# Kernel optimization log

Measured on AMD Instinct MI355X. Metric: run time of the kernel, lower is better.

Reference implementation:

```python
import jax, jax.numpy as jnp
import numpy as np

N = 128  # image size
J = 4    # number of scales
L = 4    # number of orientations


def make_morlet_filters(n, j_max, n_angles):
    """Fixed Morlet filter bank in Fourier space, shape [J, L, N, N] (real)."""
    freqs = np.fft.fftfreq(n) * 2.0 * np.pi
    kx = freqs[:, None] * np.ones((1, n))
    ky = np.ones((n, 1)) * freqs[None, :]
    filters = np.zeros((j_max, n_angles, n, n), dtype=np.float32)
    for j in range(j_max):
        k0 = 3.0 * np.pi / 4.0 / (2.0 ** j)   # central frequency of scale j
        sigma = 0.8 * (2.0 ** j)               # gaussian width in space
        for l in range(n_angles):
            theta = np.pi * l / n_angles
            k0x, k0y = k0 * np.cos(theta), k0 * np.sin(theta)
            beta = np.exp(-0.5 * sigma ** 2 * k0 ** 2)  # zero-mean correction
            g_shift = np.exp(-0.5 * sigma ** 2 * ((kx - k0x) ** 2 + (ky - k0y) ** 2))
            g_zero = np.exp(-0.5 * sigma ** 2 * (kx ** 2 + ky ** 2))
            filters[j, l] = g_shift - beta * g_zero
    return jnp.asarray(filters)


PSI = make_morlet_filters(N, J, L)  # fixed (non-learned) filter bank
VALID_PAIRS = [(j1, j2) for j1 in range(J) for j2 in range(J) if j2 > j1]  # 6 pairs


def setup_inputs() -> dict:
    key = jax.random.key(0)
    k1, k2, k3, k4, k5 = jax.random.split(key, 5)
    B = 64
    return {
        "image_batch": jax.random.normal(k1, (B, N, N), dtype=jnp.float32),
        "fc1_w": jax.random.normal(k2, (4, 11), dtype=jnp.float32) * 0.3,
        "fc1_b": jax.random.normal(k3, (4,), dtype=jnp.float32) * 0.1,
        "fc2_w": jax.random.normal(k4, (10, 4), dtype=jnp.float32) * 0.3,
        "fc2_b": jax.random.normal(k5, (10,), dtype=jnp.float32) * 0.1,
    }


def _scattering(image):
    # image: [B, N, N]
    i_hat = jnp.fft.fft2(image)  # [B,N,N] complex64
    s0 = jnp.mean(image, axis=(1, 2))  # [B]
    # first order: |x * psi_{j1,l1}|  -> [B,J,L,N,N]
    u1 = jnp.abs(jnp.fft.ifft2(i_hat[:, None, None] * PSI[None]))
    s1 = jnp.mean(u1, axis=(2, 3, 4))  # [B,J] averaged over orientations+space
    u1_hat = jnp.fft.fft2(u1)  # [B,J,L,N,N]
    # second order: only j2 > j1 (others NaN in original and masked out)
    s2_list = []
    for (j1, j2) in VALID_PAIRS:
        # [B, L1, L2, N, N]
        field = jnp.fft.ifft2(u1_hat[:, j1, :, None] * PSI[j2][None, None])
        s2_list.append(jnp.mean(jnp.abs(field), axis=(1, 2, 3, 4)))
    s2 = jnp.stack(s2_list, axis=1)  # [B,6]
    return jnp.concatenate([s0[:, None], s1, s2], axis=1)  # [B,11]


def reference(image_batch, fc1_w, fc1_b, fc2_w, fc2_b):
    coeffs = _scattering(image_batch)                      # [B,11]
    h = jax.nn.relu(coeffs @ fc1_w.T + fc1_b)              # [B,4]
    return jax.nn.sigmoid(h @ fc2_w.T + fc2_b)             # [B,10]
```

## Files before the change

kernel.cpp:

```cpp
#include <hip/hip_runtime.h>
#include <math.h>

#define NN   128
#define SS   129
#define TT   512
#define NPIX 16384
#define EPT  32
#define SG   65
#define SG32 33


__device__ __forceinline__ float2 cmul(float2 a, float2 w) {
    return make_float2(a.x * w.x - a.y * w.y, a.x * w.y + a.y * w.x);
}
__device__ __forceinline__ float2 cmulc(float2 a, float2 w) {
    return make_float2(a.x * w.x + a.y * w.y, a.y * w.x - a.x * w.y);
}

template<int SGN>
__device__ __forceinline__ void fft4(float2* f) {
    float2 t0 = make_float2(f[0].x + f[2].x, f[0].y + f[2].y);
    float2 t1 = make_float2(f[0].x - f[2].x, f[0].y - f[2].y);
    float2 t2 = make_float2(f[1].x + f[3].x, f[1].y + f[3].y);
    float2 t3 = make_float2(f[1].x - f[3].x, f[1].y - f[3].y);
    float2 t3i = (SGN > 0) ? make_float2(-t3.y, t3.x) : make_float2(t3.y, -t3.x);
    f[0] = make_float2(t0.x + t2.x, t0.y + t2.y);
    f[1] = make_float2(t1.x + t3i.x, t1.y + t3i.y);
    f[2] = make_float2(t0.x - t2.x, t0.y - t2.y);
    f[3] = make_float2(t1.x - t3i.x, t1.y - t3i.y);
}

template<int SGN>
__device__ __forceinline__ void fft8(float2* f) {
    const float R = 0.70710678118654752f;
    const float WC[4] = {1.f, R, 0.f, -R};
    const float WS[4] = {0.f, R, 1.f, R};
    #pragma unroll
    for (int stage = 0; stage < 3; ++stage) {
        const int L = 8 >> stage, half = L >> 1, step = 1 << stage;
        #pragma unroll
        for (int base = 0; base < 8; base += L) {
            #pragma unroll
            for (int j = 0; j < half; ++j) {
                float2 u = f[base + j], v = f[base + half + j];
                f[base + j] = make_float2(u.x + v.x, u.y + v.y);
                float dx = u.x - v.x, dy = u.y - v.y;
                const int t = j * step;
                const float wr = WC[t];
                const float wi = (SGN > 0) ? WS[t] : -WS[t];
                f[base + half + j] = make_float2(dx * wr - dy * wi, dx * wi + dy * wr);
            }
        }
    }
    float2 tmp;
    tmp = f[1]; f[1] = f[4]; f[4] = tmp;
    tmp = f[3]; f[3] = f[6]; f[6] = tmp;
}

template<int SGN>
__device__ __forceinline__ void fft16(float2* f) {
    const float WC[8] = {1.f, 0.92387953251f, 0.70710678119f, 0.38268343236f,
                         0.f, -0.38268343236f, -0.70710678119f, -0.92387953251f};
    const float WS[8] = {0.f, 0.38268343236f, 0.70710678119f, 0.92387953251f,
                         1.f, 0.92387953251f, 0.70710678119f, 0.38268343236f};
    #pragma unroll
    for (int stage = 0; stage < 4; ++stage) {
        const int L = 16 >> stage, half = L >> 1, step = 1 << stage;
        #pragma unroll
        for (int base = 0; base < 16; base += L) {
            #pragma unroll
            for (int j = 0; j < half; ++j) {
                float2 u = f[base + j], v = f[base + half + j];
                f[base + j] = make_float2(u.x + v.x, u.y + v.y);
                float dx = u.x - v.x, dy = u.y - v.y;
                const int t = j * step;
                const float wr = WC[t];
                const float wi = (SGN > 0) ? WS[t] : -WS[t];
                f[base + half + j] = make_float2(dx * wr - dy * wi, dx * wi + dy * wr);
            }
        }
    }
    float2 tmp;
    tmp = f[1];  f[1]  = f[8];  f[8]  = tmp;
    tmp = f[2];  f[2]  = f[4];  f[4]  = tmp;
    tmp = f[3];  f[3]  = f[12]; f[12] = tmp;
    tmp = f[5];  f[5]  = f[10]; f[10] = tmp;
    tmp = f[7];  f[7]  = f[14]; f[14] = tmp;
    tmp = f[11]; f[11] = f[13]; f[13] = tmp;
}

__device__ __forceinline__ float waveReduceSum(float v) {
    #pragma unroll
    for (int off = 32; off > 0; off >>= 1) v += __shfl_down(v, off, 64);
    return v;
}

__device__ __forceinline__ void buildTw(float2* tw, int tid) {
    if (tid < 128) {
        float s, c;
        __sincosf((float)tid * 0.04908738521234052f, &s, &c);
        tw[tid] = make_float2(c, s);
    }
}

__device__ __forceinline__ float pass32x4(float4* __restrict__ P4a,
                                          float4* __restrict__ P4b,
                                          const float2* __restrict__ tw, int tid) {
    __syncthreads();
    {
        float4* P = (tid & 256) ? P4b : P4a;
        int line = tid & 31, a = (tid >> 5) & 7;
        float2 f0[4], f1[4];
        #pragma unroll
        for (int kb = 0; kb < 4; ++kb) {
            float4 v = P[(4 * a + kb) * SG32 + line];
            f0[kb] = make_float2(v.x, v.y); f1[kb] = make_float2(v.z, v.w);
        }
        fft4<1>(f0); fft4<1>(f1);
        #pragma unroll
        for (int t = 0; t < 4; ++t) {
            float2 w = tw[4 * t * a];
            float2 aa = cmul(f0[t], w), d = cmul(f1[t], w);
            P[(4 * a + t) * SG32 + line] = make_float4(aa.x, aa.y, d.x, d.y);
        }
    }
    __syncthreads();
    if (tid < 256) {
        float4* P = (tid & 128) ? P4b : P4a;
        int line = tid & 31, t = (tid >> 5) & 3;
        float2 f0[8], f1[8];
        #pragma unroll
        for (int a = 0; a < 8; ++a) {
            float4 v = P[(4 * a + t) * SG32 + line];
            f0[a] = make_float2(v.x, v.y); f1[a] = make_float2(v.z, v.w);
        }
        fft8<1>(f0); fft8<1>(f1);
        #pragma unroll
        for (int n1 = 0; n1 < 8; ++n1)
            P[(4 * n1 + t) * SG32 + line] =
                make_float4(f0[n1].x, f0[n1].y, f1[n1].x, f1[n1].y);
    }
    __syncthreads();
    {
        float4* P = (tid & 256) ? P4b : P4a;
        int row = tid & 31, a = (tid >> 5) & 7;
        float4* R = P + row * SG32 + 4 * a;
        float2 f0[4], f1[4];
        #pragma unroll
        for (int kb = 0; kb < 4; ++kb) {
            float4 v = R[kb];
            f0[kb] = make_float2(v.x, v.y); f1[kb] = make_float2(v.z, v.w);
        }
        fft4<1>(f0); fft4<1>(f1);
        #pragma unroll
        for (int t = 0; t < 4; ++t) {
            float2 w = tw[4 * t * a];
            float2 aa = cmul(f0[t], w), d = cmul(f1[t], w);
            R[t] = make_float4(aa.x, aa.y, d.x, d.y);
        }
    }
    __syncthreads();
    float a2 = 0.f;
    if (tid < 256) {
        float4* P = (tid & 128) ? P4b : P4a;
        int row = tid & 31, t = (tid >> 5) & 3;
        float4* R = P + row * SG32 + t;
        float2 f0[8], f1[8];
        #pragma unroll
        for (int a = 0; a < 8; ++a) {
            float4 v = R[4 * a];
            f0[a] = make_float2(v.x, v.y); f1[a] = make_float2(v.z, v.w);
        }
        fft8<1>(f0); fft8<1>(f1);
        #pragma unroll
        for (int n1 = 0; n1 < 8; ++n1) {
            a2 += sqrtf(f0[n1].x * f0[n1].x + f0[n1].y * f0[n1].y);
            a2 += sqrtf(f1[n1].x * f1[n1].x + f1[n1].y * f1[n1].y);
        }
    }
    return a2;
}

__device__ __forceinline__ void pass32combo(float2* __restrict__ Q0, float2* __restrict__ Q1,
                                            float2* __restrict__ Q2, float2* __restrict__ Q3,
                                            float4* __restrict__ Pa, float4* __restrict__ Pb,
                                            const float2* __restrict__ tw, int tid,
                                            float& aq, float& ap) {
    __syncthreads();
    {
        float2* Qx = (tid & 256) ? Q2 : Q0;
        float2* Qy = (tid & 256) ? Q3 : Q1;
        float4* P  = (tid & 256) ? Pb : Pa;
        int line = tid & 31, a = (tid >> 5) & 7;
        float2 q0[4], q1[4], f0[4], f1[4];
        #pragma unroll
        for (int kb = 0; kb < 4; ++kb) {
            int o = (4 * a + kb) * SG32 + line;
            q0[kb] = Qx[o]; q1[kb] = Qy[o];
            float4 v = P[o];
            f0[kb] = make_float2(v.x, v.y); f1[kb] = make_float2(v.z, v.w);
        }
        fft4<1>(q0); fft4<1>(q1); fft4<1>(f0); fft4<1>(f1);
        #pragma unroll
        for (int t = 0; t < 4; ++t) {
            float2 w = tw[4 * t * a];
            int o = (4 * a + t) * SG32 + line;
            Qx[o] = cmul(q0[t], w); Qy[o] = cmul(q1[t], w);
            float2 aa = cmul(f0[t], w), d = cmul(f1[t], w);
            P[o] = make_float4(aa.x, aa.y, d.x, d.y);
        }
    }
    __syncthreads();
    if (tid < 256) {
        float2* Qx = (tid & 128) ? Q2 : Q0;
        float2* Qy = (tid & 128) ? Q3 : Q1;
        float4* P  = (tid & 128) ? Pb : Pa;
        int line = tid & 31, t = (tid >> 5) & 3;
        float2 q0[8], q1[8], f0[8], f1[8];
        #pragma unroll
        for (int a = 0; a < 8; ++a) {
            int o = (4 * a + t) * SG32 + line;
            q0[a] = Qx[o]; q1[a] = Qy[o];
            float4 v = P[o];
            f0[a] = make_float2(v.x, v.y); f1[a] = make_float2(v.z, v.w);
        }
        fft8<1>(q0); fft8<1>(q1); fft8<1>(f0); fft8<1>(f1);
        #pragma unroll
        for (int n1 = 0; n1 < 8; ++n1) {
            int o = (4 * n1 + t) * SG32 + line;
            Qx[o] = q0[n1]; Qy[o] = q1[n1];
            P[o] = make_float4(f0[n1].x, f0[n1].y, f1[n1].x, f1[n1].y);
        }
    }
    __syncthreads();
    {
        float2* Qx = (tid & 256) ? Q2 : Q0;
        float2* Qy = (tid & 256) ? Q3 : Q1;
        float4* P  = (tid & 256) ? Pb : Pa;
        int row = tid & 31, a = (tid >> 5) & 7;
        int base = row * SG32 + 4 * a;
        float2 q0[4], q1[4], f0[4], f1[4];
        #pragma unroll
        for (int kb = 0; kb < 4; ++kb) {
            q0[kb] = Qx[base + kb]; q1[kb] = Qy[base + kb];
            float4 v = P[base + kb];
            f0[kb] = make_float2(v.x, v.y); f1[kb] = make_float2(v.z, v.w);
        }
        fft4<1>(q0); fft4<1>(q1); fft4<1>(f0); fft4<1>(f1);
        #pragma unroll
        for (int t = 0; t < 4; ++t) {
            float2 w = tw[4 * t * a];
            Qx[base + t] = cmul(q0[t], w); Qy[base + t] = cmul(q1[t], w);
            float2 aa = cmul(f0[t], w), d = cmul(f1[t], w);
            P[base + t] = make_float4(aa.x, aa.y, d.x, d.y);
        }
    }
    __syncthreads();
    aq = 0.f; ap = 0.f;
    if (tid < 256) {
        float2* Qx = (tid & 128) ? Q2 : Q0;
        float2* Qy = (tid & 128) ? Q3 : Q1;
        float4* P  = (tid & 128) ? Pb : Pa;
        int row = tid & 31, t = (tid >> 5) & 3;
        int base = row * SG32 + t;
        float2 q0[8], q1[8], f0[8], f1[8];
        #pragma unroll
        for (int a = 0; a < 8; ++a) {
            int o = base + 4 * a;
            q0[a] = Qx[o]; q1[a] = Qy[o];
            float4 v = P[o];
            f0[a] = make_float2(v.x, v.y); f1[a] = make_float2(v.z, v.w);
        }
        fft8<1>(q0); fft8<1>(q1); fft8<1>(f0); fft8<1>(f1);
        #pragma unroll
        for (int n1 = 0; n1 < 8; ++n1) {
            aq += sqrtf(q0[n1].x * q0[n1].x + q0[n1].y * q0[n1].y);
            aq += sqrtf(q1[n1].x * q1[n1].x + q1[n1].y * q1[n1].y);
            ap += sqrtf(f0[n1].x * f0[n1].x + f0[n1].y * f0[n1].y);
            ap += sqrtf(f1[n1].x * f1[n1].x + f1[n1].y * f1[n1].y);
        }
    }
}

template<int ES, int LS>
__device__ __forceinline__ void fwdA(float2* __restrict__ F,
                                     const float2* __restrict__ tw, int tid) {
    #pragma unroll
    for (int i = 0; i < 4; ++i) {
        int u = i * TT + tid;
        int t = u >> 7, x = u & 127;
        float2* M = F + x * LS;
        float2 f[8];
        #pragma unroll
        for (int n1 = 0; n1 < 8; ++n1) f[n1] = M[(t + 16 * n1) * ES];
        fft8<-1>(f);
        #pragma unroll
        for (int ka = 0; ka < 8; ++ka)
            M[(t + 16 * ka) * ES] = cmulc(f[ka], tw[t * ka]);
    }
}

template<int ES, int LS>
__device__ __forceinline__ void fwdB(float2* __restrict__ F, int tid) {
    #pragma unroll
    for (int i = 0; i < 2; ++i) {
        int u = i * TT + tid;
        int ka = u >> 7, x = u & 127;
        float2* M = F + x * LS;
        float2 g[16];
        #pragma unroll
        for (int t = 0; t < 16; ++t) g[t] = M[(16 * ka + t) * ES];
        fft16<-1>(g);
        #pragma unroll
        for (int kb = 0; kb < 16; ++kb) M[(16 * ka + kb) * ES] = g[kb];
    }
}

__device__ __forceinline__ void fwdB_col_capture(const float2* __restrict__ F, int tid,
                                                 float2* __restrict__ uh) {
    #pragma unroll
    for (int i = 0; i < 2; ++i) {
        int u = i * TT + tid;
        int ka = u >> 7, c = u & 127;
        float2 g[16];
        #pragma unroll
        for (int t = 0; t < 16; ++t) g[t] = F[(16 * ka + t) * SS + c];
        fft16<-1>(g);
        #pragma unroll
        for (int kb = 0; kb < 16; ++kb) uh[i * 16 + kb] = g[kb];
    }
}

template<int ES, int LS>
__device__ __forceinline__ void invA(float2* __restrict__ F,
                                     const float2* __restrict__ tw, int tid) {
    #pragma unroll
    for (int i = 0; i < 2; ++i) {
        int u = i * TT + tid;
        int ka = u >> 7, x = u & 127;
        float2* M = F + x * LS;
        float2 g[16];
        #pragma unroll
        for (int kb = 0; kb < 16; ++kb) g[kb] = M[(16 * ka + kb) * ES];
        fft16<1>(g);
        #pragma unroll
        for (int t = 0; t < 16; ++t)
            M[(16 * ka + t) * ES] = cmul(g[t], tw[t * ka]);
    }
}

template<int ES, int LS>
__device__ __forceinline__ void invB(float2* __restrict__ F, int tid) {
    #pragma unroll
    for (int i = 0; i < 4; ++i) {
        int u = i * TT + tid;
        int t = u >> 7, x = u & 127;
        float2* M = F + x * LS;
        float2 f[8];
        #pragma unroll
        for (int ka = 0; ka < 8; ++ka) f[ka] = M[(16 * ka + t) * ES];
        fft8<1>(f);
        #pragma unroll
        for (int nh = 0; nh < 8; ++nh) M[(t + 16 * nh) * ES] = f[nh];
    }
}

__device__ __forceinline__ void invBmag_fwdA_row(float2* __restrict__ F,
                                                 const float2* __restrict__ tw,
                                                 int tid, float& acc) {
    #pragma unroll
    for (int i = 0; i < 4; ++i) {
        int u = i * TT + tid;
        int t = u >> 7, x = u & 127;
        float2* M = F + x * SS;
        float2 f[8];
        #pragma unroll
        for (int ka = 0; ka < 8; ++ka) f[ka] = M[16 * ka + t];
        fft8<1>(f);
        #pragma unroll
        for (int nh = 0; nh < 8; ++nh) {
            float m = sqrtf(f[nh].x * f[nh].x + f[nh].y * f[nh].y);
            acc += m;
            f[nh] = make_float2(m, 0.f);
        }
        fft8<-1>(f);
        #pragma unroll
        for (int ka = 0; ka < 8; ++ka)
            M[t + 16 * ka] = cmulc(f[ka], tw[t * ka]);
    }
}

__global__ __attribute__((amdgpu_flat_work_group_size(TT, TT), amdgpu_waves_per_eu(2, 2)))
void k_pre(const float* __restrict__ img,
           float* __restrict__ psi,
           float2* __restrict__ ihat,
           float* __restrict__ coeffs) {
    __shared__ float2 F[NN * SS];
    __shared__ float2 tw[128];
    __shared__ float red[TT / 64];
    int blk = blockIdx.x, tid = threadIdx.x;
    if (blk >= 64) {
        if (blk == 80) {
            for (int i = tid; i < 64 * 11; i += TT)
                if (i % 11 != 0) coeffs[i] = 0.f;
            return;
        }
        int f = blk - 64;
        int j = f >> 2, l = f & 3;
        float k0    = 2.35619449019234493f / (float)(1 << j);
        float sigma = 0.8f * (float)(1 << j);
        float s2    = sigma * sigma;
        float theta = 0.78539816339744831f * (float)l;
        float k0x = k0 * cosf(theta);
        float k0y = k0 * sinf(theta);
        float beta = expf(-0.5f * s2 * k0 * k0);
        const float FSTEP = 0.04908738521234052f;
        float* dst = psi + (size_t)f * NPIX;
        for (int i = tid; i < NPIX; i += TT) {
            int pr = i >> 7, pc = i & 127;
            int kr = (pr >> 4) + 8 * (pr & 15);
            int kc = (pc >> 4) + 8 * (pc & 15);
            float fr = (float)(kr < 64 ? kr : kr - 128) * FSTEP;
            float fc = (float)(kc < 64 ? kc : kc - 128) * FSTEP;
            float dx = fr - k0x, dy = fc - k0y;
            float g1 = expf(-0.5f * s2 * (dx * dx + dy * dy));
            float g0 = expf(-0.5f * s2 * (fr * fr + fc * fc));
            dst[i] = g1 - beta * g0;
        }
        return;
    }
    int b = blk;
    buildTw(tw, tid);
    const float* im = img + (size_t)b * NPIX;
    float acc = 0.f;
    #pragma unroll
    for (int k = 0; k < EPT; ++k) {
        int e = k * TT + tid;
        float v = im[e];
        acc += v;
        F[(e >> 7) * SS + (e & 127)] = make_float2(v, 0.f);
    }
    float ws = waveReduceSum(acc);
    if ((tid & 63) == 0) red[tid >> 6] = ws;
    __syncthreads();
    if (tid == 0) {
        float t = 0.f;
        #pragma unroll
        for (int w = 0; w < TT / 64; ++w) t += red[w];
        coeffs[b * 11 + 0] = t * (1.f / 16384.f);
    }
    fwdA<1, SS>(F, tw, tid);  __syncthreads();
    fwdB<1, SS>(F, tid);      __syncthreads();
    fwdA<SS, 1>(F, tw, tid);  __syncthreads();
    float2 uh[32];
    fwdB_col_capture(F, tid, uh);
    float2* dst = ihat + (size_t)b * NPIX;
    #pragma unroll
    for (int i = 0; i < 2; ++i) {
        int u = i * TT + tid;
        int ka = u >> 7, c = u & 127;
        #pragma unroll
        for (int kb = 0; kb < 16; ++kb)
            dst[(16 * ka + kb) * NN + c] = uh[i * 16 + kb];
    }
}

__global__ __attribute__((amdgpu_flat_work_group_size(TT, TT), amdgpu_waves_per_eu(2, 2)))
void k_scat_big(const float2* __restrict__ ihat,
                const float* __restrict__ psi,
                float* __restrict__ coeffs) {
    __shared__ __align__(16) float2 F[16640];
    __shared__ float2 tw[128];
    float2* G2a = F;
    float2* G2b = F + 4160;
    float2* G2c = F + 8320;
    float2* G2d = F + 12480;
    float2* Q0 = F;
    float2* Q1 = F + 1056;
    float2* Q2 = F + 2112;
    float2* Q3 = F + 3168;
    float4* Pa = (float4*)(F + 4224);
    float4* Pb = (float4*)(F + 6336);
    int tid = threadIdx.x;
    int x = blockIdx.x;
    int b = x & 63, l1 = x >> 6;
    const float2* ih = ihat + (size_t)b * NPIX;
    const float*  p1 = psi + (size_t)l1 * NPIX;
    buildTw(tw, tid);

    const float S1_128 = 9.3132257461547852e-10f;
    const float S2TR   = 5.6843418860808015e-14f;
    const float S2_03  = 2.2737367544323206e-13f;

    int kalo = tid >> 7, c = tid & 127;
    {
        #pragma unroll
        for (int i = 0; i < 2; ++i) {
            int ka = kalo + 4 * i;
            float2 g[16];
            #pragma unroll
            for (int kb = 0; kb < 16; ++kb) {
                int e = (16 * ka + kb) * NN + c;
                float2 z = ih[e];
                float  p = p1[e];
                g[kb] = make_float2(z.x * p, z.y * p);
            }
            fft16<1>(g);
            #pragma unroll
            for (int t = 0; t < 16; ++t)
                F[(16 * ka + t) * SS + c] = cmul(g[t], tw[t * ka]);
        }
    }
    __syncthreads();
    invB<SS, 1>(F, tid);      __syncthreads();
    invA<1, SS>(F, tw, tid);  __syncthreads();
    float acc = 0.f;
    invBmag_fwdA_row(F, tw, tid, acc);
    float ws1 = waveReduceSum(acc);
    if ((tid & 63) == 0) atomicAdd(&coeffs[b * 11 + 1], ws1 * S1_128);
    __syncthreads();
    fwdB<1, SS>(F, tid);      __syncthreads();
    fwdA<SS, 1>(F, tw, tid);  __syncthreads();
    float2 uh[32];
    fwdB_col_capture(F, tid, uh);
    __syncthreads();

    int m = c & 15;
    int fc = (c >> 4) + 8 * (c & 15);

    {
        const int ORW[4] = {21, 15, 0, -15};
        const int OCW[4] = { 0, 15, 21,  15};
        bool ckw[4]; int pcw[4];
        #pragma unroll
        for (int w = 0; w < 4; ++w) {
            int dc = (fc - OCW[w]) & 127;
            ckw[w] = (dc < 32) || (dc >= 96);
            int uc = (dc < 32) ? dc : (dc - 64);
            pcw[w] = 8 * (uc & 7) + (uc >> 3);
        }
        #pragma unroll
        for (int i = 0; i < 2; ++i) {
            int ka = kalo + 4 * i;
            #pragma unroll
            for (int kb = 0; kb < 16; ++kb) {
                int fr = ka + 8 * kb;
                float2 z = uh[i * 16 + kb];
                int e = (16 * ka + kb) * NN + c;
                #pragma unroll
                for (int w = 0; w < 4; ++w) {
                    if (ckw[w]) {
                        int dr = (fr - ORW[w]) & 127;
                        if (dr < 32 || dr >= 96) {
                            int ur = (dr < 32) ? dr : (dr - 64);
                            int pr = 8 * (ur & 7) + (ur >> 3);
                            float pv = psi[(size_t)(4 + w) * NPIX + e];
                            float2* G = (w == 0) ? G2a : (w == 1) ? G2b
                                       : (w == 2) ? G2c : G2d;
                            G[pr * SG + pcw[w]] = make_float2(z.x * pv, z.y * pv);
                        }
                    }
                }
            }
        }
        __syncthreads();
        {
            int col = tid & 63, k8 = tid >> 6;
            float2 f0[8], f1[8], f2[8], f3[8];
            #pragma unroll
            for (int kb = 0; kb < 8; ++kb) {
                int o = (8 * k8 + kb) * SG + col;
                f0[kb] = G2a[o]; f1[kb] = G2b[o]; f2[kb] = G2c[o]; f3[kb] = G2d[o];
            }
            fft8<1>(f0); fft8<1>(f1); fft8<1>(f2); fft8<1>(f3);
            #pragma unroll
            for (int q = 0; q < 8; ++q) {
                float2 w = tw[2 * q * k8];
                int o = (8 * k8 + q) * SG + col;
                G2a[o] = cmul(f0[q], w); G2b[o] = cmul(f1[q], w);
                G2c[o] = cmul(f2[q], w); G2d[o] = cmul(f3[q], w);
            }
        }
        __syncthreads();
        {
            int col = tid & 63, q = tid >> 6;
            float2 f0[8], f1[8], f2[8], f3[8];
            #pragma unroll
            for (int k8 = 0; k8 < 8; ++k8) {
                int o = (8 * k8 + q) * SG + col;
                f0[k8] = G2a[o]; f1[k8] = G2b[o]; f2[k8] = G2c[o]; f3[k8] = G2d[o];
            }
            fft8<1>(f0); fft8<1>(f1); fft8<1>(f2); fft8<1>(f3);
            #pragma unroll
            for (int n1 = 0; n1 < 8; ++n1) {
                int o = (8 * n1 + q) * SG + col;
                G2a[o] = f0[n1]; G2b[o] = f1[n1]; G2c[o] = f2[n1]; G2d[o] = f3[n1];
            }
        }
        __syncthreads();
        {
            int row = tid & 63, k8 = tid >> 6;
            int base = row * SG + 8 * k8;
            float2 f0[8], f1[8], f2[8], f3[8];
            #pragma unroll
            for (int kb = 0; kb < 8; ++kb) {
                f0[kb] = G2a[base + kb]; f1[kb] = G2b[base + kb];
                f2[kb] = G2c[base + kb]; f3[kb] = G2d[base + kb];
            }
            fft8<1>(f0); fft8<1>(f1); fft8<1>(f2); fft8<1>(f3);
            #pragma unroll
            for (int q = 0; q < 8; ++q) {
                float2 w = tw[2 * q * k8];
                G2a[base + q] = cmul(f0[q], w); G2b[base + q] = cmul(f1[q], w);
                G2c[base + q] = cmul(f2[q], w); G2d[base + q] = cmul(f3[q], w);
            }
        }
        __syncthreads();
        float a2 = 0.f;
        {
            int row = tid & 63, q = tid >> 6;
            int base = row * SG + q;
            float2 f0[8], f1[8], f2[8], f3[8];
            #pragma unroll
            for (int k8 = 0; k8 < 8; ++k8) {
                int o = base + 8 * k8;
                f0[k8] = G2a[o]; f1[k8] = G2b[o]; f2[k8] = G2c[o]; f3[k8] = G2d[o];
            }
            fft8<1>(f0); fft8<1>(f1); fft8<1>(f2); fft8<1>(f3);
            #pragma unroll
            for (int n1 = 0; n1 < 8; ++n1) {
                a2 += sqrtf(f0[n1].x * f0[n1].x + f0[n1].y * f0[n1].y);
                a2 += sqrtf(f1[n1].x * f1[n1].x + f1[n1].y * f1[n1].y);
                a2 += sqrtf(f2[n1].x * f2[n1].x + f2[n1].y * f2[n1].y);
                a2 += sqrtf(f3[n1].x * f3[n1].x + f3[n1].y * f3[n1].y);
            }
        }
        float ws2 = waveReduceSum(a2);
        if ((tid & 63) == 0) atomicAdd(&coeffs[b * 11 + 5 + 0], ws2 * S2TR);
        __syncthreads();
    }

    {
        const int OR2[4] = {9, 6, 0, -6};
        const int OC2[4] = {0, 6, 9,  6};
        bool ckq[4]; int pcq[4];
        #pragma unroll
        for (int w = 0; w < 4; ++w) {
            int dc = (fc - OC2[w]) & 127;
            ckq[w] = (dc < 16) || (dc >= 112);
            int f32c = (dc < 16) ? dc : (dc - 96);
            pcq[w] = 4 * (f32c & 7) + (f32c >> 3);
        }
        bool ck32 = (m < 2) || (m >= 14);
        int pc32 = 4 * (c >> 4) + ((m < 2) ? m : (m - 12));
        const float* p30 = psi + (size_t)12 * NPIX;
        #pragma unroll
        for (int i = 0; i < 2; ++i) {
            int ka = kalo + 4 * i;
            #pragma unroll
            for (int kb = 0; kb < 16; ++kb) {
                int fr = ka + 8 * kb;
                float2 z = uh[i * 16 + kb];
                int e = (16 * ka + kb) * NN + c;
                #pragma unroll
                for (int w = 0; w < 4; ++w) {
                    if (ckq[w]) {
                        int dr = (fr - OR2[w]) & 127;
                        if (dr < 16 || dr >= 112) {
                            int f32r = (dr < 16) ? dr : (dr - 96);
                            int pr = 4 * (f32r & 7) + (f32r >> 3);
                            float pv = psi[(size_t)(8 + w) * NPIX + e];
                            float2* Q = (w == 0) ? Q0 : (w == 1) ? Q1
                                       : (w == 2) ? Q2 : Q3;
                            Q[pr * SG32 + pcq[w]] = make_float2(z.x * pv, z.y * pv);
                        }
                    }
                }
                if (ck32 && (kb < 2 || kb >= 14)) {
                    int pr32 = 4 * ka + ((kb < 2) ? kb : (kb - 12));
                    float a0 = p30[e], a1 = p30[NPIX + e];
                    float a2f = p30[2 * NPIX + e], a3 = p30[3 * NPIX + e];
                    Pa[pr32 * SG32 + pc32] =
                        make_float4(z.x * a0, z.y * a0, z.x * a1, z.y * a1);
                    Pb[pr32 * SG32 + pc32] =
                        make_float4(z.x * a2f, z.y * a2f, z.x * a3, z.y * a3);
                }
            }
        }
        float aq, ap;
        pass32combo(Q0, Q1, Q2, Q3, Pa, Pb, tw, tid, aq, ap);
        float wsq = waveReduceSum(aq);
        float wsp = waveReduceSum(ap);
        if ((tid & 63) == 0) {
            atomicAdd(&coeffs[b * 11 + 5 + 1], wsq * S2_03);
            atomicAdd(&coeffs[b * 11 + 5 + 2], wsp * S2_03);
        }
    }
}

__global__ __attribute__((amdgpu_flat_work_group_size(TT, TT), amdgpu_waves_per_eu(4, 4)))
void k_scat_small(const float2* __restrict__ ihat,
                  const float* __restrict__ psi,
                  float* __restrict__ coeffs) {
    __shared__ __align__(16) float2 S[8448];
    __shared__ float2 tw[128];
    float2* G2  = S;
    float2* G32 = S;
    float4* P4a = (float4*)S;
    float4* P4b = (float4*)S + 1056;
    float2* Qs0 = S;
    float2* Qs1 = S + 1056;
    float2* Qs2 = S + 2112;
    float2* Qs3 = S + 3168;
    float4* Psa = (float4*)(S + 4224);
    float4* Psb = (float4*)(S + 6336);
    float2* H32 = S + 6144;
    int tid = threadIdx.x;
    int x = blockIdx.x;
    int b = x & 63, l1 = (x >> 6) & 3;
    int t0 = x >> 8;
    int j1 = (t0 == 0) ? 1 : (t0 + 1);
    const float2* ih = ihat + (size_t)b * NPIX;
    const float*  p1 = psi + (size_t)(j1 * 4 + l1) * NPIX;
    buildTw(tw, tid);

    const float S1_64 = 3.7252902984619141e-9f;
    const float S1_32 = 1.4901161193847656e-8f;
    const float S2_32 = 9.0949470177292824e-13f;

    int kalo = tid >> 7, c = tid & 127;

    if (t0 == 0) {
        const int OR1[4] = {21, 15, 0, -15};
        const int OC1[4] = { 0, 15, 21,  15};
        int fc = (c >> 4) + 8 * (c & 15);
        int dc = (fc - OC1[l1]) & 127;
        bool ck = (dc < 32) || (dc >= 96);
        int ucw = (dc < 32) ? dc : (dc - 64);
        int pcd = 8 * (ucw & 7) + (ucw >> 3);
        if (ck) {
            #pragma unroll
            for (int i = 0; i < 2; ++i) {
                int ka = kalo + 4 * i;
                #pragma unroll
                for (int kb = 0; kb < 16; ++kb) {
                    int fr = ka + 8 * kb;
                    int dr = (fr - OR1[l1]) & 127;
                    if (dr < 32 || dr >= 96) {
                        int ur = (dr < 32) ? dr : (dr - 64);
                        int pr = 8 * (ur & 7) + (ur >> 3);
                        int e = (16 * ka + kb) * NN + c;
                        float2 z = ih[e];
                        float  p = p1[e];
                        G2[pr * SG + pcd] = make_float2(z.x * p, z.y * p);
                    }
                }
            }
        }
        __syncthreads();
        {
            int col = tid & 63, k8 = tid >> 6;
            float2 f[8];
            #pragma unroll
            for (int kb = 0; kb < 8; ++kb) f[kb] = G2[(8 * k8 + kb) * SG + col];
            fft8<1>(f);
            #pragma unroll
            for (int q = 0; q < 8; ++q)
                G2[(8 * k8 + q) * SG + col] = cmul(f[q], tw[2 * q * k8]);
        }
        __syncthreads();
        {
            int col = tid & 63, q = tid >> 6;
            float2 f[8];
            #pragma unroll
            for (int k8 = 0; k8 < 8; ++k8) f[k8] = G2[(8 * k8 + q) * SG + col];
            fft8<1>(f);
            #pragma unroll
            for (int n1 = 0; n1 < 8; ++n1) G2[(8 * n1 + q) * SG + col] = f[n1];
        }
        __syncthreads();
        {
            int row = tid & 63, k8 = tid >> 6;
            float2* R = G2 + row * SG + 8 * k8;
            float2 f[8];
            #pragma unroll
            for (int kb = 0; kb < 8; ++kb) f[kb] = R[kb];
            fft8<1>(f);
            #pragma unroll
            for (int q = 0; q < 8; ++q) R[q] = cmul(f[q], tw[2 * q * k8]);
        }
        __syncthreads();
        float acc = 0.f;
        {
            int row = tid & 63, q = tid >> 6;
            float2* R = G2 + row * SG + q;
            float2 f[8];
            #pragma unroll
            for (int k8 = 0; k8 < 8; ++k8) f[k8] = R[8 * k8];
            fft8<1>(f);
            #pragma unroll
            for (int n1 = 0; n1 < 8; ++n1) {
                float mg = sqrtf(f[n1].x * f[n1].x + f[n1].y * f[n1].y);
                acc += mg;
                f[n1] = make_float2(mg, 0.f);
            }
            fft8<-1>(f);
            #pragma unroll
            for (int ka = 0; ka < 8; ++ka)
                R[8 * ka] = cmulc(f[ka], tw[2 * q * ka]);
        }
        float ws1 = waveReduceSum(acc);
        if ((tid & 63) == 0) atomicAdd(&coeffs[b * 11 + 2], ws1 * S1_64);
        __syncthreads();
        {
            int row2 = tid & 63, ka = tid >> 6;
            float2* R2 = G2 + row2 * SG + 8 * ka;
            float2 g[8];
            #pragma unroll
            for (int t = 0; t < 8; ++t) g[t] = R2[t];
            fft8<-1>(g);
            #pragma unroll
            for (int kb = 0; kb < 8; ++kb) R2[kb] = g[kb];
        }
        __syncthreads();
        {
            int col = tid & 63, t = tid >> 6;
            float2 g[8];
            #pragma unroll
            for (int n1 = 0; n1 < 8; ++n1) g[n1] = G2[(t + 8 * n1) * SG + col];
            fft8<-1>(g);
            #pragma unroll
            for (int ka = 0; ka < 8; ++ka)
                G2[(t + 8 * ka) * SG + col] = cmulc(g[ka], tw[2 * t * ka]);
        }
        __syncthreads();
        float2 vh[8];
        int c6 = tid & 63, ka8 = tid >> 6;
        {
            float2 g[8];
            #pragma unroll
            for (int t = 0; t < 8; ++t) g[t] = G2[(8 * ka8 + t) * SG + c6];
            fft8<-1>(g);
            #pragma unroll
            for (int kb = 0; kb < 8; ++kb) vh[kb] = g[kb];
        }
        __syncthreads();

        int uc64 = 8 * (c6 & 7) + (c6 >> 3);
        int fc128 = (uc64 < 32) ? uc64 : (uc64 + 64);
        int scI = 16 * (fc128 & 7) + (fc128 >> 3);
        int se[8];
        #pragma unroll
        for (int kb = 0; kb < 8; ++kb) {
            int ur = 8 * kb + ka8;
            int fr128 = (ur < 32) ? ur : (ur + 64);
            se[kb] = (16 * (fr128 & 7) + (fr128 >> 3)) * NN + scI;
        }

        {
            const int OR2[4] = {9, 6, 0, -6};
            const int OC2[4] = {0, 6, 9,  6};
            bool ckq[4]; int pcq[4];
            #pragma unroll
            for (int w = 0; w < 4; ++w) {
                int dcw = (uc64 - OC2[w]) & 63;
                ckq[w] = (dcw < 16) || (dcw >= 48);
                int f32c = (dcw < 16) ? dcw : (dcw - 32);
                pcq[w] = 4 * (f32c & 7) + (f32c >> 3);
            }
            int m6 = c6 & 7;
            bool ckV = (m6 < 2) || (m6 >= 6);
            int p32c = 4 * (c6 >> 3) + ((m6 < 2) ? m6 : (m6 - 4));
            const float* p30 = psi + (size_t)12 * NPIX;
            #pragma unroll
            for (int kb = 0; kb < 8; ++kb) {
                int ur = 8 * kb + ka8;
                float2 z = vh[kb];
                int e = se[kb];
                #pragma unroll
                for (int w = 0; w < 4; ++w) {
                    if (ckq[w]) {
                        int dr = (ur - OR2[w]) & 63;
                        if (dr < 16 || dr >= 48) {
                            int f32r = (dr < 16) ? dr : (dr - 32);
                            int pr = 4 * (f32r & 7) + (f32r >> 3);
                            float pv = psi[(size_t)(8 + w) * NPIX + e];
                            float2* Q = (w == 0) ? Qs0 : (w == 1) ? Qs1
                                       : (w == 2) ? Qs2 : Qs3;
                            Q[pr * SG32 + pcq[w]] = make_float2(z.x * pv, z.y * pv);
                        }
                    }
                }
                if (ckV && (kb < 2 || kb >= 6)) {
                    int pr32 = 4 * ka8 + (kb & 3);
                    float a0 = p30[e], a1 = p30[NPIX + e];
                    float a2f = p30[2 * NPIX + e], a3 = p30[3 * NPIX + e];
                    Psa[pr32 * SG32 + p32c] =
                        make_float4(z.x * a0, z.y * a0, z.x * a1, z.y * a1);
                    Psb[pr32 * SG32 + p32c] =
                        make_float4(z.x * a2f, z.y * a2f, z.x * a3, z.y * a3);
                }
            }
            float aq, ap;
            pass32combo(Qs0, Qs1, Qs2, Qs3, Psa, Psb, tw, tid, aq, ap);
            float wsq = waveReduceSum(aq);
            float wsp = waveReduceSum(ap);
            if ((tid & 63) == 0) {
                atomicAdd(&coeffs[b * 11 + 5 + 3], wsq * S2_32);
                atomicAdd(&coeffs[b * 11 + 5 + 4], wsp * S2_32);
            }
        }
        return;
    }

    if (t0 == 2) {
        int m = c & 15;
        bool ck32 = (m < 2) || (m >= 14);
        int pc32 = 4 * (c >> 4) + ((m < 2) ? m : (m - 12));
        if (ck32) {
            #pragma unroll
            for (int i = 0; i < 2; ++i) {
                int ka = kalo + 4 * i;
                #pragma unroll
                for (int kb = 0; kb < 16; ++kb) {
                    if (kb < 2 || kb >= 14) {
                        int e = (16 * ka + kb) * NN + c;
                        float2 z = ih[e];
                        float  p = p1[e];
                        int pr32 = 4 * ka + ((kb < 2) ? kb : (kb - 12));
                        G32[pr32 * SG32 + pc32] = make_float2(z.x * p, z.y * p);
                    }
                }
            }
        }
        __syncthreads();
        if (tid < 256) {
            int line = tid & 31, a = tid >> 5;
            float2 f[4];
            #pragma unroll
            for (int kb = 0; kb < 4; ++kb) f[kb] = G32[(4 * a + kb) * SG32 + line];
            fft4<1>(f);
            #pragma unroll
            for (int t = 0; t < 4; ++t)
                G32[(4 * a + t) * SG32 + line] = cmul(f[t], tw[4 * t * a]);
        }
        __syncthreads();
        if (tid < 128) {
            int line = tid & 31, t = tid >> 5;
            float2 f[8];
            #pragma unroll
            for (int a = 0; a < 8; ++a) f[a] = G32[(4 * a + t) * SG32 + line];
            fft8<1>(f);
            #pragma unroll
            for (int n1 = 0; n1 < 8; ++n1) G32[(4 * n1 + t) * SG32 + line] = f[n1];
        }
        __syncthreads();
        if (tid < 256) {
            int row = tid & 31, a = tid >> 5;
            float2* R = G32 + row * SG32 + 4 * a;
            float2 f[4];
            #pragma unroll
            for (int kb = 0; kb < 4; ++kb) f[kb] = R[kb];
            fft4<1>(f);
            #pragma unroll
            for (int t = 0; t < 4; ++t) R[t] = cmul(f[t], tw[4 * t * a]);
        }
        __syncthreads();
        float acc = 0.f;
        if (tid < 128) {
            int row = tid & 31, t = tid >> 5;
            float2* R = G32 + row * SG32 + t;
            float2 f[8];
            #pragma unroll
            for (int a = 0; a < 8; ++a) f[a] = R[4 * a];
            fft8<1>(f);
            #pragma unroll
            for (int n1 = 0; n1 < 8; ++n1)
                acc += sqrtf(f[n1].x * f[n1].x + f[n1].y * f[n1].y);
        }
        float ws1 = waveReduceSum(acc);
        if ((tid & 63) == 0 && tid < 128) atomicAdd(&coeffs[b * 11 + 4], ws1 * S1_32);
        return;
    }

    int m = c & 15;
    bool colKeep = (m < 4) || (m >= 12);
    if (colKeep) {
        #pragma unroll
        for (int i = 0; i < 2; ++i) {
            int ka = kalo + 4 * i;
            #pragma unroll
            for (int kb = 0; kb < 16; ++kb) {
                if (kb < 4 || kb >= 12) {
                    int e = (16 * ka + kb) * NN + c;
                    float2 z = ih[e];
                    float  p = p1[e];
                    int pr64 = 8 * ka + ((kb < 4) ? kb : (kb - 8));
                    int pc64 = 8 * (c >> 4) + ((m < 4) ? m : (m - 8));
                    G2[pr64 * SG + pc64] = make_float2(z.x * p, z.y * p);
                }
            }
        }
    }
    __syncthreads();
    {
        int col = tid & 63, k8 = tid >> 6;
        float2 f[8];
        #pragma unroll
        for (int kb = 0; kb < 8; ++kb) f[kb] = G2[(8 * k8 + kb) * SG + col];
        fft8<1>(f);
        #pragma unroll
        for (int q = 0; q < 8; ++q)
            G2[(8 * k8 + q) * SG + col] = cmul(f[q], tw[2 * q * k8]);
    }
    __syncthreads();
    {
        int col = tid & 63, q = tid >> 6;
        float2 f[8];
        #pragma unroll
        for (int k8 = 0; k8 < 8; ++k8) f[k8] = G2[(8 * k8 + q) * SG + col];
        fft8<1>(f);
        #pragma unroll
        for (int n1 = 0; n1 < 8; ++n1) G2[(8 * n1 + q) * SG + col] = f[n1];
    }
    __syncthreads();
    {
        int row = tid & 63, k8 = tid >> 6;
        float2* R = G2 + row * SG + 8 * k8;
        float2 f[8];
        #pragma unroll
        for (int kb = 0; kb < 8; ++kb) f[kb] = R[kb];
        fft8<1>(f);
        #pragma unroll
        for (int q = 0; q < 8; ++q) R[q] = cmul(f[q], tw[2 * q * k8]);
    }
    __syncthreads();
    float acc = 0.f;
    {
        int row = tid & 63, q = tid >> 6;
        float2* R = G2 + row * SG + q;
        float2 f[8];
        #pragma unroll
        for (int k8 = 0; k8 < 8; ++k8) f[k8] = R[8 * k8];
        fft8<1>(f);
        #pragma unroll
        for (int n1 = 0; n1 < 8; ++n1) {
            float mg = sqrtf(f[n1].x * f[n1].x + f[n1].y * f[n1].y);
            acc += mg;
            f[n1] = make_float2(mg, 0.f);
        }
        fft8<-1>(f);
        #pragma unroll
        for (int ka = 0; ka < 8; ++ka)
            R[8 * ka] = cmulc(f[ka], tw[2 * q * ka]);
    }
    float ws1 = waveReduceSum(acc);
    if ((tid & 63) == 0) atomicAdd(&coeffs[b * 11 + 3], ws1 * S1_64);
    __syncthreads();
    {
        int row2 = tid & 63, ka = tid >> 6;
        float2* R2 = G2 + row2 * SG + 8 * ka;
        float2 g[8];
        #pragma unroll
        for (int t = 0; t < 8; ++t) g[t] = R2[t];
        fft8<-1>(g);
        #pragma unroll
        for (int kb = 0; kb < 8; ++kb) R2[kb] = g[kb];
    }
    __syncthreads();
    {
        int col = tid & 63, t = tid >> 6;
        float2 g[8];
        #pragma unroll
        for (int n1 = 0; n1 < 8; ++n1) g[n1] = G2[(t + 8 * n1) * SG + col];
        fft8<-1>(g);
        #pragma unroll
        for (int ka = 0; ka < 8; ++ka)
            G2[(t + 8 * ka) * SG + col] = cmulc(g[ka], tw[2 * t * ka]);
    }
    __syncthreads();
    {
        int col = tid & 63, ka = tid >> 6;
        float2 g[8];
        #pragma unroll
        for (int t = 0; t < 8; ++t) g[t] = G2[(8 * ka + t) * SG + col];
        fft8<-1>(g);
        int br = col & 7, ar = col >> 3;
        if (br < 2 || br >= 6) {
            int p32row = 4 * ar + (br & 3);
            #pragma unroll
            for (int kb = 0; kb < 8; ++kb) {
                if (kb < 2 || kb >= 6)
                    H32[(4 * ka + (kb & 3)) * 32 + p32row] = g[kb];
            }
        }
    }
    __syncthreads();

    {
        bool ck32 = (m < 2) || (m >= 14);
        int pc32 = 4 * (c >> 4) + ((m < 2) ? m : (m - 12));
        const float* p0 = psi + (size_t)12 * NPIX;
        const float* pq1 = p0 + NPIX;
        const float* pq2 = pq1 + NPIX;
        const float* pq3 = pq2 + NPIX;
        if (ck32) {
            #pragma unroll
            for (int i = 0; i < 2; ++i) {
                int ka = kalo + 4 * i;
                #pragma unroll
                for (int kb = 0; kb < 16; ++kb) {
                    if (kb < 2 || kb >= 14) {
                        int pr32 = 4 * ka + ((kb < 2) ? kb : (kb - 12));
                        float2 z = H32[pr32 * 32 + pc32];
                        int e = (16 * ka + kb) * NN + c;
                        float a0 = p0[e], a1 = pq1[e], a2f = pq2[e], a3 = pq3[e];
                        P4a[pr32 * SG32 + pc32] =
                            make_float4(z.x * a0, z.y * a0, z.x * a1, z.y * a1);
                        P4b[pr32 * SG32 + pc32] =
                            make_float4(z.x * a2f, z.y * a2f, z.x * a3, z.y * a3);
                    }
                }
            }
        }
        float a2 = pass32x4(P4a, P4b, tw, tid);
        float ws2 = waveReduceSum(a2);
        if ((tid & 63) == 0) atomicAdd(&coeffs[b * 11 + 5 + 5], ws2 * S2_32);
    }
}

__global__ void k_mlp(const float* __restrict__ coeffs,
                      const float* __restrict__ w1, const float* __restrict__ b1,
                      const float* __restrict__ w2, const float* __restrict__ b2,
                      float* __restrict__ out) {
    int b = threadIdx.x;
    if (b >= 64) return;
    float c[11];
    #pragma unroll
    for (int i = 0; i < 11; ++i) c[i] = coeffs[b * 11 + i];
    float h[4];
    #pragma unroll
    for (int k = 0; k < 4; ++k) {
        float s = b1[k];
        #pragma unroll
        for (int i = 0; i < 11; ++i) s += w1[k * 11 + i] * c[i];
        h[k] = fmaxf(s, 0.f);
    }
    #pragma unroll
    for (int o = 0; o < 10; ++o) {
        float s = b2[o];
        #pragma unroll
        for (int k = 0; k < 4; ++k) s += w2[o * 4 + k] * h[k];
        out[b * 10 + o] = 1.f / (1.f + expf(-s));
    }
}

extern "C" void kernel_launch(void* const* d_in, const int* in_sizes, int n_in,
                              void* d_out, int out_size, void* d_ws, size_t ws_size,
                              hipStream_t stream) {
    const float* img = (const float*)d_in[0];
    const float* w1  = (const float*)d_in[1];
    const float* b1  = (const float*)d_in[2];
    const float* w2  = (const float*)d_in[3];
    const float* b2  = (const float*)d_in[4];
    float* out = (float*)d_out;

    float*  ws     = (float*)d_ws;
    float*  psi    = ws;
    float2* ihat   = (float2*)(ws + 16 * NPIX);
    float*  coeffs = ws + 16 * NPIX + 2 * 64 * NPIX;

    hipLaunchKernelGGL(k_pre,        dim3(81),  dim3(TT), 0, stream, img, psi, ihat, coeffs);
    hipLaunchKernelGGL(k_scat_big,   dim3(256), dim3(TT), 0, stream, ihat, psi, coeffs);
    hipLaunchKernelGGL(k_scat_small, dim3(768), dim3(TT), 0, stream, ihat, psi, coeffs);
    hipLaunchKernelGGL(k_mlp,        dim3(1),   dim3(64), 0, stream, coeffs, w1, b1, w2, b2, out);
}
```

Baseline: 182.6 us.

## Split image FFT into row and column kernels and use 64x64 pass for j2=2

The single 64-block forward FFT pre-kernel becomes two kernels, each running 256 blocks over 32-row or 32-column strips. Row FFTs are staged through global memory between them, which spreads the initial FFT across more CUs. The mean coefficient s0 now comes from the DC bin of the FFT, so the separate reduction is gone. In k_scat_big, the second-order j2=2 pair switches from four shifted 32x32 windows to one 64x64 cropped window processing all four orientations together, trading extra FFT work for simpler scatter and fewer bank conflicts.

```diff
diff --git a/kernel.cpp b/kernel.cpp
--- a/kernel.cpp
+++ b/kernel.cpp
@@ -391,21 +391,19 @@
 }
 
 __global__ __attribute__((amdgpu_flat_work_group_size(TT, TT), amdgpu_waves_per_eu(2, 2)))
-void k_pre(const float* __restrict__ img,
-           float* __restrict__ psi,
-           float2* __restrict__ ihat,
-           float* __restrict__ coeffs) {
-    __shared__ float2 F[NN * SS];
+void k_pre1(const float* __restrict__ img,
+            float* __restrict__ psi,
+            float2* __restrict__ interm,
+            float* __restrict__ coeffs) {
+    __shared__ __align__(16) float2 F[32 * SS];
     __shared__ float2 tw[128];
-    __shared__ float red[TT / 64];
     int blk = blockIdx.x, tid = threadIdx.x;
-    if (blk >= 64) {
-        if (blk == 80) {
-            for (int i = tid; i < 64 * 11; i += TT)
-                if (i % 11 != 0) coeffs[i] = 0.f;
+    if (blk >= 256) {
+        if (blk == 272) {
+            for (int i = tid; i < 64 * 11; i += TT) coeffs[i] = 0.f;
             return;
         }
-        int f = blk - 64;
+        int f = blk - 256;
         int j = f >> 2, l = f & 3;
         float k0    = 2.35619449019234493f / (float)(1 << j);
         float sigma = 0.8f * (float)(1 << j);
@@ -429,39 +427,85 @@
         }
         return;
     }
-    int b = blk;
+    int b = blk >> 2, q = blk & 3;
     buildTw(tw, tid);
-    const float* im = img + (size_t)b * NPIX;
-    float acc = 0.f;
-    #pragma unroll
-    for (int k = 0; k < EPT; ++k) {
+    const float* im = img + (size_t)b * NPIX + (size_t)q * 32 * NN;
+    #pragma unroll
+    for (int k = 0; k < 8; ++k) {
         int e = k * TT + tid;
-        float v = im[e];
-        acc += v;
-        F[(e >> 7) * SS + (e & 127)] = make_float2(v, 0.f);
-    }
-    float ws = waveReduceSum(acc);
-    if ((tid & 63) == 0) red[tid >> 6] = ws;
-    __syncthreads();
-    if (tid == 0) {
-        float t = 0.f;
-        #pragma unroll
-        for (int w = 0; w < TT / 64; ++w) t += red[w];
-        coeffs[b * 11 + 0] = t * (1.f / 16384.f);
-    }
-    fwdA<1, SS>(F, tw, tid);  __syncthreads();
-    fwdB<1, SS>(F, tid);      __syncthreads();
-    fwdA<SS, 1>(F, tw, tid);  __syncthreads();
-    float2 uh[32];
-    fwdB_col_capture(F, tid, uh);
-    float2* dst = ihat + (size_t)b * NPIX;
-    #pragma unroll
-    for (int i = 0; i < 2; ++i) {
-        int u = i * TT + tid;
-        int ka = u >> 7, c = u & 127;
+        F[(e >> 7) * SS + (e & 127)] = make_float2(im[e], 0.f);
+    }
+    __syncthreads();
+    {
+        int x = tid & 31, t = tid >> 5;
+        float2* M = F + x * SS;
+        float2 f[8];
+        #pragma unroll
+        for (int n1 = 0; n1 < 8; ++n1) f[n1] = M[t + 16 * n1];
+        fft8<-1>(f);
+        #pragma unroll
+        for (int ka = 0; ka < 8; ++ka)
+            M[t + 16 * ka] = cmulc(f[ka], tw[t * ka]);
+    }
+    __syncthreads();
+    if (tid < 256) {
+        int x = tid & 31, ka = tid >> 5;
+        float2* M = F + x * SS + 16 * ka;
+        float2 g[16];
+        #pragma unroll
+        for (int t = 0; t < 16; ++t) g[t] = M[t];
+        fft16<-1>(g);
+        #pragma unroll
+        for (int kb = 0; kb < 16; ++kb) M[kb] = g[kb];
+    }
+    __syncthreads();
+    float2* dst = interm + (size_t)b * NPIX + (size_t)q * 32 * NN;
+    #pragma unroll
+    for (int k = 0; k < 8; ++k) {
+        int e = k * TT + tid;
+        dst[e] = F[(e >> 7) * SS + (e & 127)];
+    }
+}
+
+__global__ __attribute__((amdgpu_flat_work_group_size(TT, TT), amdgpu_waves_per_eu(2, 2)))
+void k_pre2(float2* __restrict__ ihat,
+            float* __restrict__ coeffs) {
+    __shared__ __align__(16) float2 F[128 * 33];
+    __shared__ float2 tw[128];
+    int blk = blockIdx.x, tid = threadIdx.x;
+    int b = blk >> 2, q = blk & 3;
+    buildTw(tw, tid);
+    float2* base = ihat + (size_t)b * NPIX + q * 32;
+    #pragma unroll
+    for (int k = 0; k < 8; ++k) {
+        int e = k * TT + tid;
+        int r = e >> 5, cl = e & 31;
+        F[r * 33 + cl] = base[r * NN + cl];
+    }
+    __syncthreads();
+    {
+        int cl = tid & 31, t = tid >> 5;
+        float2 f[8];
+        #pragma unroll
+        for (int n1 = 0; n1 < 8; ++n1) f[n1] = F[(t + 16 * n1) * 33 + cl];
+        fft8<-1>(f);
+        #pragma unroll
+        for (int ka = 0; ka < 8; ++ka)
+            F[(t + 16 * ka) * 33 + cl] = cmulc(f[ka], tw[t * ka]);
+    }
+    __syncthreads();
+    if (tid < 256) {
+        int cl = tid & 31, ka = tid >> 5;
+        float2 g[16];
+        #pragma unroll
+        for (int t = 0; t < 16; ++t) g[t] = F[(16 * ka + t) * 33 + cl];
+        fft16<-1>(g);
+        float2* dst = base + cl;
         #pragma unroll
         for (int kb = 0; kb < 16; ++kb)
-            dst[(16 * ka + kb) * NN + c] = uh[i * 16 + kb];
+            dst[(16 * ka + kb) * NN] = g[kb];
+        if (q == 0 && cl == 0 && ka == 0)
+            coeffs[b * 11 + 0] = g[0].x * (1.f / 16384.f);
     }
 }
 
@@ -471,16 +515,14 @@
                 float* __restrict__ coeffs) {
     __shared__ __align__(16) float2 F[16640];
     __shared__ float2 tw[128];
+    float4* G4a = (float4*)F;
+    float4* G4b = (float4*)(F + 8320);
     float2* G2a = F;
     float2* G2b = F + 4160;
     float2* G2c = F + 8320;
     float2* G2d = F + 12480;
-    float2* Q0 = F;
-    float2* Q1 = F + 1056;
-    float2* Q2 = F + 2112;
-    float2* Q3 = F + 3168;
-    float4* Pa = (float4*)(F + 4224);
-    float4* Pb = (float4*)(F + 6336);
+    float4* P4a = (float4*)F;
+    float4* P4b = (float4*)F + 1056;
     int tid = threadIdx.x;
     int x = blockIdx.x;
     int b = x & 63, l1 = x >> 6;
@@ -526,6 +568,8 @@
     __syncthreads();
 
     int m = c & 15;
+    bool colKeep = (m < 4) || (m >= 12);
+    int pc64 = 8 * (c >> 4) + ((m < 4) ? m : (m - 8));
     int fc = (c >> 4) + 8 * (c & 15);
 
     {
@@ -641,60 +685,150 @@
     }
 
     {
-        const int OR2[4] = {9, 6, 0, -6};
-        const int OC2[4] = {0, 6, 9,  6};
-        bool ckq[4]; int pcq[4];
-        #pragma unroll
-        for (int w = 0; w < 4; ++w) {
-            int dc = (fc - OC2[w]) & 127;
-            ckq[w] = (dc < 16) || (dc >= 112);
-            int f32c = (dc < 16) ? dc : (dc - 96);
-            pcq[w] = 4 * (f32c & 7) + (f32c >> 3);
-        }
+        const float* p0 = psi + (size_t)8 * NPIX;
+        const float* pq1 = p0 + NPIX;
+        const float* pq2 = pq1 + NPIX;
+        const float* pq3 = pq2 + NPIX;
+        if (colKeep) {
+            #pragma unroll
+            for (int i = 0; i < 2; ++i) {
+                int ka = kalo + 4 * i;
+                #pragma unroll
+                for (int kb = 0; kb < 16; ++kb) {
+                    if (kb < 4 || kb >= 12) {
+                        int pr64 = 8 * ka + ((kb < 4) ? kb : (kb - 8));
+                        float2 z = uh[i * 16 + kb];
+                        int e = (16 * ka + kb) * NN + c;
+                        float a0 = p0[e], a1 = pq1[e], a2f = pq2[e], a3 = pq3[e];
+                        G4a[pr64 * SG + pc64] =
+                            make_float4(z.x * a0, z.y * a0, z.x * a1, z.y * a1);
+                        G4b[pr64 * SG + pc64] =
+                            make_float4(z.x * a2f, z.y * a2f, z.x * a3, z.y * a3);
+                    }
+                }
+            }
+        }
+        __syncthreads();
+        {
+            int col = tid & 63, k8 = tid >> 6;
+            float2 f0[8], f1[8], f2[8], f3[8];
+            #pragma unroll
+            for (int kb = 0; kb < 8; ++kb) {
+                int o = (8 * k8 + kb) * SG + col;
+                float4 v = G4a[o];
+                f0[kb] = make_float2(v.x, v.y); f1[kb] = make_float2(v.z, v.w);
+                float4 u = G4b[o];
+                f2[kb] = make_float2(u.x, u.y); f3[kb] = make_float2(u.z, u.w);
+            }
+            fft8<1>(f0); fft8<1>(f1); fft8<1>(f2); fft8<1>(f3);
+            #pragma unroll
+            for (int q = 0; q < 8; ++q) {
+                float2 w = tw[2 * q * k8];
+                int o = (8 * k8 + q) * SG + col;
+                float2 a = cmul(f0[q], w), d = cmul(f1[q], w);
+                G4a[o] = make_float4(a.x, a.y, d.x, d.y);
+                float2 a2c = cmul(f2[q], w), d2 = cmul(f3[q], w);
+                G4b[o] = make_float4(a2c.x, a2c.y, d2.x, d2.y);
+            }
+        }
+        __syncthreads();
+        {
+            int col = tid & 63, q = tid >> 6;
+            float2 f0[8], f1[8], f2[8], f3[8];
+            #pragma unroll
+            for (int k8 = 0; k8 < 8; ++k8) {
+                int o = (8 * k8 + q) * SG + col;
+                float4 v = G4a[o];
+                f0[k8] = make_float2(v.x, v.y); f1[k8] = make_float2(v.z, v.w);
+                float4 u = G4b[o];
+                f2[k8] = make_float2(u.x, u.y); f3[k8] = make_float2(u.z, u.w);
+            }
+            fft8<1>(f0); fft8<1>(f1); fft8<1>(f2); fft8<1>(f3);
+            #pragma unroll
+            for (int n1 = 0; n1 < 8; ++n1) {
+                int o = (8 * n1 + q) * SG + col;
+                G4a[o] = make_float4(f0[n1].x, f0[n1].y, f1[n1].x, f1[n1].y);
+                G4b[o] = make_float4(f2[n1].x, f2[n1].y, f3[n1].x, f3[n1].y);
+            }
+        }
+        __syncthreads();
+        {
+            int row = tid & 63, k8 = tid >> 6;
+            int base = row * SG + 8 * k8;
+            float2 f0[8], f1[8], f2[8], f3[8];
+            #pragma unroll
+            for (int kb = 0; kb < 8; ++kb) {
+                float4 v = G4a[base + kb];
+                f0[kb] = make_float2(v.x, v.y); f1[kb] = make_float2(v.z, v.w);
+                float4 u = G4b[base + kb];
+                f2[kb] = make_float2(u.x, u.y); f3[kb] = make_float2(u.z, u.w);
+            }
+            fft8<1>(f0); fft8<1>(f1); fft8<1>(f2); fft8<1>(f3);
+            #pragma unroll
+            for (int q = 0; q < 8; ++q) {
+                float2 w = tw[2 * q * k8];
+                float2 a = cmul(f0[q], w), d = cmul(f1[q], w);
+                G4a[base + q] = make_float4(a.x, a.y, d.x, d.y);
+                float2 a2c = cmul(f2[q], w), d2 = cmul(f3[q], w);
+                G4b[base + q] = make_float4(a2c.x, a2c.y, d2.x, d2.y);
+            }
+        }
+        __syncthreads();
+        float a2 = 0.f;
+        {
+            int row = tid & 63, q = tid >> 6;
+            int base = row * SG + q;
+            float2 f0[8], f1[8], f2[8], f3[8];
+            #pragma unroll
+            for (int k8 = 0; k8 < 8; ++k8) {
+                float4 v = G4a[base + 8 * k8];
+                f0[k8] = make_float2(v.x, v.y); f1[k8] = make_float2(v.z, v.w);
+                float4 u = G4b[base + 8 * k8];
+                f2[k8] = make_float2(u.x, u.y); f3[k8] = make_float2(u.z, u.w);
+            }
+            fft8<1>(f0); fft8<1>(f1); fft8<1>(f2); fft8<1>(f3);
+            #pragma unroll
+            for (int n1 = 0; n1 < 8; ++n1) {
+                a2 += sqrtf(f0[n1].x * f0[n1].x + f0[n1].y * f0[n1].y);
+                a2 += sqrtf(f1[n1].x * f1[n1].x + f1[n1].y * f1[n1].y);
+                a2 += sqrtf(f2[n1].x * f2[n1].x + f2[n1].y * f2[n1].y);
+                a2 += sqrtf(f3[n1].x * f3[n1].x + f3[n1].y * f3[n1].y);
+            }
+        }
+        float ws2 = waveReduceSum(a2);
+        if ((tid & 63) == 0) atomicAdd(&coeffs[b * 11 + 5 + 1], ws2 * S2TR);
+        __syncthreads();
+    }
+
+    {
         bool ck32 = (m < 2) || (m >= 14);
         int pc32 = 4 * (c >> 4) + ((m < 2) ? m : (m - 12));
-        const float* p30 = psi + (size_t)12 * NPIX;
-        #pragma unroll
-        for (int i = 0; i < 2; ++i) {
-            int ka = kalo + 4 * i;
-            #pragma unroll
-            for (int kb = 0; kb < 16; ++kb) {
-                int fr = ka + 8 * kb;
-                float2 z = uh[i * 16 + kb];
-                int e = (16 * ka + kb) * NN + c;
+        const float* p0 = psi + (size_t)12 * NPIX;
+        const float* pq1 = p0 + NPIX;
+        const float* pq2 = pq1 + NPIX;
+        const float* pq3 = pq2 + NPIX;
+        if (ck32) {
+            #pragma unroll
+            for (int i = 0; i < 2; ++i) {
+                int ka = kalo + 4 * i;
                 #pragma unroll
-                for (int w = 0; w < 4; ++w) {
-                    if (ckq[w]) {
-                        int dr = (fr - OR2[w]) & 127;
-                        if (dr < 16 || dr >= 112) {
-                            int f32r = (dr < 16) ? dr : (dr - 96);
-                            int pr = 4 * (f32r & 7) + (f32r >> 3);
-                            float pv = psi[(size_t)(8 + w) * NPIX + e];
-                            float2* Q = (w == 0) ? Q0 : (w == 1) ? Q1
-                                       : (w == 2) ? Q2 : Q3;
-                            Q[pr * SG32 + pcq[w]] = make_float2(z.x * pv, z.y * pv);
-                        }
+                for (int kb = 0; kb < 16; ++kb) {
+                    if (kb < 2 || kb >= 14) {
+                        int pr32 = 4 * ka + ((kb < 2) ? kb : (kb - 12));
+                        float2 z = uh[i * 16 + kb];
+                        int e = (16 * ka + kb) * NN + c;
+                        float a0 = p0[e], a1 = pq1[e], a2f = pq2[e], a3 = pq3[e];
+                        P4a[pr32 * SG32 + pc32] =
+                            make_float4(z.x * a0, z.y * a0, z.x * a1, z.y * a1);
+                        P4b[pr32 * SG32 + pc32] =
+                            make_float4(z.x * a2f, z.y * a2f, z.x * a3, z.y * a3);
                     }
                 }
-                if (ck32 && (kb < 2 || kb >= 14)) {
-                    int pr32 = 4 * ka + ((kb < 2) ? kb : (kb - 12));
-                    float a0 = p30[e], a1 = p30[NPIX + e];
-                    float a2f = p30[2 * NPIX + e], a3 = p30[3 * NPIX + e];
-                    Pa[pr32 * SG32 + pc32] =
-                        make_float4(z.x * a0, z.y * a0, z.x * a1, z.y * a1);
-                    Pb[pr32 * SG32 + pc32] =
-                        make_float4(z.x * a2f, z.y * a2f, z.x * a3, z.y * a3);
-                }
-            }
-        }
-        float aq, ap;
-        pass32combo(Q0, Q1, Q2, Q3, Pa, Pb, tw, tid, aq, ap);
-        float wsq = waveReduceSum(aq);
-        float wsp = waveReduceSum(ap);
-        if ((tid & 63) == 0) {
-            atomicAdd(&coeffs[b * 11 + 5 + 1], wsq * S2_03);
-            atomicAdd(&coeffs[b * 11 + 5 + 2], wsp * S2_03);
-        }
+            }
+        }
+        float a2 = pass32x4(P4a, P4b, tw, tid);
+        float ws2 = waveReduceSum(a2);
+        if ((tid & 63) == 0) atomicAdd(&coeffs[b * 11 + 5 + 2], ws2 * S2_03);
     }
 }
 
@@ -1170,7 +1304,8 @@
     float2* ihat   = (float2*)(ws + 16 * NPIX);
     float*  coeffs = ws + 16 * NPIX + 2 * 64 * NPIX;
 
-    hipLaunchKernelGGL(k_pre,        dim3(81),  dim3(TT), 0, stream, img, psi, ihat, coeffs);
+    hipLaunchKernelGGL(k_pre1,       dim3(273), dim3(TT), 0, stream, img, psi, ihat, coeffs);
+    hipLaunchKernelGGL(k_pre2,       dim3(256), dim3(TT), 0, stream, ihat, coeffs);
     hipLaunchKernelGGL(k_scat_big,   dim3(256), dim3(TT), 0, stream, ihat, psi, coeffs);
     hipLaunchKernelGGL(k_scat_small, dim3(768), dim3(TT), 0, stream, ihat, psi, coeffs);
     hipLaunchKernelGGL(k_mlp,        dim3(1),   dim3(64), 0, stream, coeffs, w1, b1, w2, b2, out);
```

Result: faster. 177.3 us (-2.9%).
